# Performance work log

Measured on AMD Instinct MI355X. Metric: run time of the kernel, lower is better.

Reference implementation:

```python
import jax, jax.numpy as jnp
import numpy as np

L = 4      # num_decoders
D = 512    # d (model dim)
F = 512    # f (attention dim; must equal D for residual adds)
V = 32000  # vocab_size
S = 2048   # sequence length
EPS = 1e-5


def layer_norm(x, g, b):
    mu = jnp.mean(x, axis=-1, keepdims=True)
    var = jnp.var(x, axis=-1, keepdims=True)
    return (x - mu) * jax.lax.rsqrt(var + EPS) * g + b


def setup_inputs() -> dict:
    key = jax.random.key(0)
    ks = jax.random.split(key, 20)
    s = 0.02
    n = jax.random.normal
    return {
        "x":   n(ks[0], (S, D), jnp.float32),
        "Wq":  n(ks[1], (L, D, F), jnp.float32) * s,
        "bq":  jnp.zeros((L, F), jnp.float32),
        "Wk":  n(ks[2], (L, D, F), jnp.float32) * s,
        "bk":  jnp.zeros((L, F), jnp.float32),
        "Wv":  n(ks[3], (L, D, F), jnp.float32) * s,
        "bv":  jnp.zeros((L, F), jnp.float32),
        "Wp":  n(ks[4], (L, F, F), jnp.float32) * s,
        "bp":  jnp.zeros((L, F), jnp.float32),
        "g1":  1.0 + n(ks[5], (L, F), jnp.float32) * s,
        "be1": n(ks[6], (L, F), jnp.float32) * s,
        "W1":  n(ks[7], (L, F, 4 * F), jnp.float32) * s,
        "b1":  jnp.zeros((L, 4 * F), jnp.float32),
        "W2":  n(ks[8], (L, 4 * F, D), jnp.float32) * s,
        "b2":  jnp.zeros((L, D), jnp.float32),
        "g2":  1.0 + n(ks[9], (L, D), jnp.float32) * s,
        "be2": n(ks[10], (L, D), jnp.float32) * s,
        "Wf":  n(ks[11], (D, V), jnp.float32) * s,
        "bf":  jnp.zeros((V,), jnp.float32),
    }


def reference(x, Wq, bq, Wk, bk, Wv, bv, Wp, bp, g1, be1, W1, b1, W2, b2, g2, be2, Wf, bf):
    seq = x.shape[0]
    scale = 1.0 / jnp.sqrt(jnp.asarray(F, x.dtype))
    # causal mask: position i attends to j <= i (intended triu masking)
    causal = jnp.tril(jnp.ones((seq, seq), dtype=bool))
    neg_inf = jnp.asarray(-jnp.inf, x.dtype)
    for l in range(L):
        res = jax.lax.stop_gradient(x)  # original uses x.detach().clone()
        q = x @ Wq[l] + bq[l]
        k = x @ Wk[l] + bk[l]
        v = x @ Wv[l] + bv[l]
        scores = (q @ k.T) * scale                      # [S, S]
        scores = jnp.where(causal, scores, neg_inf)
        att = jax.nn.softmax(scores, axis=1)
        z = (att @ v) @ Wp[l] + bp[l]
        x = layer_norm(z + res, g1[l], be1[l])
        res = jax.lax.stop_gradient(x)
        h = x @ W1[l] + b1[l]                           # no activation in original FFN
        h = h @ W2[l] + b2[l]
        x = layer_norm(h + res, g2[l], be2[l])
    logits = x @ Wf + bf                                # [S, V]
    return jax.nn.softmax(logits, axis=1)
```

## Files before the change

### kernel.cpp

```cpp
#include <hip/hip_runtime.h>
#include <cmath>

#define SEQ 2048
#define DIM 512
#define FDIM 512
#define HDIM 2048
#define VOCAB 32000
#define NLAYER 4
#define LNEPS 1e-5f

typedef unsigned short ushort_t;
typedef __attribute__((ext_vector_type(8))) short short8;
typedef __attribute__((ext_vector_type(4))) float f32x4;

__device__ __forceinline__ ushort_t f2bf(float x) {
    union { float f; unsigned int u; } a; a.f = x;
    unsigned int r = a.u + 0x7fffu + ((a.u >> 16) & 1u);
    return (ushort_t)(r >> 16);
}
__device__ __forceinline__ float bf2f(ushort_t b) {
    union { unsigned int u; float f; } a; a.u = ((unsigned int)b) << 16; return a.f;
}

__device__ __forceinline__ void gload_lds16(const ushort_t* g, ushort_t* l) {
    __builtin_amdgcn_global_load_lds(
        (const __attribute__((address_space(1))) void*)g,
        (__attribute__((address_space(3))) void*)l, 16, 0, 0);
}

#define GEMM_CORE(AH, AL, BH, BL, LDA, LDB, KSTEPS, KBASE, TM, TN)                 \
    __shared__ ushort_t lds[16384];                                                \
    ushort_t* ldsAh = lds;                                                         \
    ushort_t* ldsAl = lds + 4096;                                                  \
    ushort_t* ldsBh = lds + 8192;                                                  \
    ushort_t* ldsBl = lds + 12288;                                                 \
    const int tid  = threadIdx.x;                                                  \
    const int lane = tid & 63, wv = tid >> 6;                                      \
    const int wm = wv >> 1, wn = wv & 1;                                           \
    const int q = lane >> 4, mlo = lane & 15;                                      \
    const int tm = (TM), tn = (TN);                                                \
    f32x4 acc[4][4];                                                               \
    _Pragma("unroll")                                                              \
    for (int i = 0; i < 4; i++)                                                    \
        _Pragma("unroll")                                                          \
        for (int j = 0; j < 4; j++)                                                \
            acc[i][j] = (f32x4){0.f, 0.f, 0.f, 0.f};                               \
    for (int ks = 0; ks < (KSTEPS); ks++) {                                        \
        const int k0 = (KBASE) + (ks << 5);                                        \
        _Pragma("unroll")                                                          \
        for (int r = 0; r < 2; r++) {                                              \
            const int c  = (r << 8) + (wv << 6) + lane;                            \
            const int i  = c & 127, kb = c >> 7;                                   \
            const int lofs = ((r << 8) + (wv << 6)) << 3;                          \
            const size_t aoff = (size_t)(tm + i) * (LDA) + k0 + (kb << 3);         \
            const size_t boff = (size_t)(tn + i) * (LDB) + k0 + (kb << 3);         \
            gload_lds16((AH) + aoff, ldsAh + lofs);                                \
            gload_lds16((AL) + aoff, ldsAl + lofs);                                \
            gload_lds16((BH) + boff, ldsBh + lofs);                                \
            gload_lds16((BL) + boff, ldsBl + lofs);                                \
        }                                                                          \
        __syncthreads();                                                           \
        short8 ah[4], al[4], bh[4], bl[4];                                         \
        _Pragma("unroll")                                                          \
        for (int t = 0; t < 4; t++) {                                              \
            const int ma = ((q << 7) + (wm << 6) + (t << 4) + mlo) << 3;           \
            const int nb = ((q << 7) + (wn << 6) + (t << 4) + mlo) << 3;           \
            ah[t] = *(const short8*)&ldsAh[ma];                                    \
            al[t] = *(const short8*)&ldsAl[ma];                                    \
            bh[t] = *(const short8*)&ldsBh[nb];                                    \
            bl[t] = *(const short8*)&ldsBl[nb];                                    \
        }                                                                          \
        _Pragma("unroll")                                                          \
        for (int i = 0; i < 4; i++)                                                \
            _Pragma("unroll")                                                      \
            for (int j = 0; j < 4; j++) {                                          \
                acc[i][j] = __builtin_amdgcn_mfma_f32_16x16x32_bf16(ah[i], bh[j], acc[i][j], 0, 0, 0); \
                acc[i][j] = __builtin_amdgcn_mfma_f32_16x16x32_bf16(ah[i], bl[j], acc[i][j], 0, 0, 0); \
                acc[i][j] = __builtin_amdgcn_mfma_f32_16x16x32_bf16(al[i], bh[j], acc[i][j], 0, 0, 0); \
            }                                                                      \
        __syncthreads();                                                           \
    }

__global__ __launch_bounds__(256) void gemm_bf16x3_k(
    const ushort_t* __restrict__ Ah, const ushort_t* __restrict__ Al,
    const ushort_t* __restrict__ Bh, const ushort_t* __restrict__ Bl,
    const float* __restrict__ bias, float* __restrict__ C,
    int K, int lda, int ldb, int ldc, float scale, int splitk, int flags,
    int bsA, int bsB, int bsC, int bsBias, int bsPart)
{
    const int bz = blockIdx.z;
    const int l  = bz / splitk, zz = bz - l * splitk;
    Ah += (size_t)l * bsA; Al += (size_t)l * bsA;
    Bh += (size_t)l * bsB; Bl += (size_t)l * bsB;
    C  += (size_t)l * bsC;
    if (bias != nullptr) bias += (size_t)l * bsBias;
    int bx = blockIdx.x, by = blockIdx.y;
    if (flags & 4) { const int t = bx; bx = by; by = t; }
    const int tmq = by << 7, tnq = bx << 7;
    if ((flags & 1) && tnq > tmq + 127) return;
    int ksteps = (K >> 5) / splitk;
    const int kbase = zz * ksteps * 32;
    if (flags & 2) {
        const int rem = (tmq + 128 - kbase) >> 5;
        if (rem < ksteps) ksteps = rem;
        if (ksteps <= 0) return;
    }
    GEMM_CORE(Ah, Al, Bh, Bl, lda, ldb, ksteps, kbase, tmq, tnq)
    const bool addb = (bias != nullptr) && (zz == 0);
    float* Cw = C + ((splitk > 1 && bsPart) ? (size_t)zz * bsPart : 0);
#pragma unroll
    for (int ti = 0; ti < 4; ti++)
#pragma unroll
        for (int tj = 0; tj < 4; tj++) {
            const int col = tn + (wn << 6) + (tj << 4) + mlo;
            const float bb = addb ? bias[col] : 0.f;
#pragma unroll
            for (int r = 0; r < 4; r++) {
                const int row = tm + (wm << 6) + (ti << 4) + (q << 2) + r;
                const float v = acc[ti][tj][r] * scale + bb;
                if (splitk == 1 || bsPart) Cw[(size_t)row * ldc + col] = v;
                else atomicAdd(&C[(size_t)row * ldc + col], v);
            }
        }
}

__global__ __launch_bounds__(256) void gemm_qkv_k(
    const ushort_t* __restrict__ Ah, const ushort_t* __restrict__ Al,
    const ushort_t* __restrict__ Bh, const ushort_t* __restrict__ Bl,
    const float* __restrict__ bias,
    ushort_t* __restrict__ QKh, ushort_t* __restrict__ QKl,
    ushort_t* __restrict__ Vh,  ushort_t* __restrict__ Vl)
{
    GEMM_CORE(Ah, Al, Bh, Bl, DIM, DIM, (DIM >> 5), 0,
              (int)(blockIdx.y << 7), (int)(blockIdx.x << 7))
#pragma unroll
    for (int ti = 0; ti < 4; ti++)
#pragma unroll
        for (int tj = 0; tj < 4; tj++) {
            const int col = tn + (wn << 6) + (tj << 4) + mlo;
            const float bb = bias[col];
#pragma unroll
            for (int r = 0; r < 4; r++) {
                const int row = tm + (wm << 6) + (ti << 4) + (q << 2) + r;
                const float v = acc[ti][tj][r] + bb;
                const ushort_t h = f2bf(v);
                const ushort_t lo = f2bf(v - bf2f(h));
                if (col < 1024) {
                    QKh[(size_t)row * 1024 + col] = h;
                    QKl[(size_t)row * 1024 + col] = lo;
                } else {
                    Vh[(size_t)(col - 1024) * SEQ + row] = h;
                    Vl[(size_t)(col - 1024) * SEQ + row] = lo;
                }
            }
        }
}

__global__ __launch_bounds__(128) void split_k(
    const float* __restrict__ src, int ld, int C,
    ushort_t* __restrict__ dh, ushort_t* __restrict__ dl)
{
    const int row = blockIdx.y;
    const int c4 = ((blockIdx.x << 7) + threadIdx.x) << 2;
    if (c4 >= C) return;
    const float4 v = *(const float4*)&src[(size_t)row * ld + c4];
    ushort_t h[4], l[4];
    const float f[4] = {v.x, v.y, v.z, v.w};
#pragma unroll
    for (int i = 0; i < 4; i++) {
        h[i] = f2bf(f[i]);
        l[i] = f2bf(f[i] - bf2f(h[i]));
    }
    *(ushort4*)&dh[(size_t)row * C + c4] = make_ushort4(h[0], h[1], h[2], h[3]);
    *(ushort4*)&dl[(size_t)row * C + c4] = make_ushort4(l[0], l[1], l[2], l[3]);
}

__global__ __launch_bounds__(128) void split_b_k(
    const float* __restrict__ src0, int ld, int C, int sbs,
    ushort_t* __restrict__ dh0, ushort_t* __restrict__ dl0, int dbs)
{
    const int lz = blockIdx.z;
    const float* src = src0 + (size_t)lz * sbs;
    ushort_t* dh = dh0 + (size_t)lz * dbs;
    ushort_t* dl = dl0 + (size_t)lz * dbs;
    const int row = blockIdx.y;
    const int c4 = ((blockIdx.x << 7) + threadIdx.x) << 2;
    if (c4 >= C) return;
    const float4 v = *(const float4*)&src[(size_t)row * ld + c4];
    ushort_t h[4], l[4];
    const float f[4] = {v.x, v.y, v.z, v.w};
#pragma unroll
    for (int i = 0; i < 4; i++) {
        h[i] = f2bf(f[i]);
        l[i] = f2bf(f[i] - bf2f(h[i]));
    }
    *(ushort4*)&dh[(size_t)row * C + c4] = make_ushort4(h[0], h[1], h[2], h[3]);
    *(ushort4*)&dl[(size_t)row * C + c4] = make_ushort4(l[0], l[1], l[2], l[3]);
}

__global__ __launch_bounds__(256) void tsplit_k(
    const float* __restrict__ src, int ld, int R,
    ushort_t* __restrict__ dh, ushort_t* __restrict__ dl)
{
    __shared__ float t[32][33];
    const int c = threadIdx.x & 31, r8 = threadIdx.x >> 5;
    const int bx = blockIdx.x, by = blockIdx.y;
#pragma unroll
    for (int i = 0; i < 4; i++) {
        const int r = (r8 << 2) + i;
        t[r][c] = src[(size_t)((by << 5) + r) * ld + (bx << 5) + c];
    }
    __syncthreads();
#pragma unroll
    for (int i = 0; i < 4; i++) {
        const int rr = (r8 << 2) + i;
        const float v = t[c][rr];
        const ushort_t h = f2bf(v);
        const ushort_t l = f2bf(v - bf2f(h));
        const size_t o = (size_t)((bx << 5) + rr) * R + (by << 5) + c;
        dh[o] = h; dl[o] = l;
    }
}

__global__ __launch_bounds__(256) void tsplit_b_k(
    const float* __restrict__ src0, int ld, int R, int sbs,
    ushort_t* __restrict__ dh0, ushort_t* __restrict__ dl0, int dbs)
{
    const int lz = blockIdx.z;
    const float* src = src0 + (size_t)lz * sbs;
    ushort_t* dh = dh0 + (size_t)lz * dbs;
    ushort_t* dl = dl0 + (size_t)lz * dbs;
    __shared__ float t[32][33];
    const int c = threadIdx.x & 31, r8 = threadIdx.x >> 5;
    const int bx = blockIdx.x, by = blockIdx.y;
#pragma unroll
    for (int i = 0; i < 4; i++) {
        const int r = (r8 << 2) + i;
        t[r][c] = src[(size_t)((by << 5) + r) * ld + (bx << 5) + c];
    }
    __syncthreads();
#pragma unroll
    for (int i = 0; i < 4; i++) {
        const int rr = (r8 << 2) + i;
        const float v = t[c][rr];
        const ushort_t h = f2bf(v);
        const ushort_t l = f2bf(v - bf2f(h));
        const size_t o = (size_t)((bx << 5) + rr) * R + (by << 5) + c;
        dh[o] = h; dl[o] = l;
    }
}

__global__ void gatherqkv_k(const float* bq, const float* bk, const float* bvp, float* d)
{
    const int i = blockIdx.x * 256 + threadIdx.x;
    if (i >= NLAYER * 1536) return;
    const int l = i / 1536, j = i - l * 1536;
    float v;
    if (j < 512)       v = bq[l * 512 + j];
    else if (j < 1024) v = bk[l * 512 + j - 512];
    else               v = bvp[l * 512 + j - 1024];
    d[i] = v;
}

__global__ __launch_bounds__(256) void bvecg_k(
    const float* __restrict__ vec, const float* __restrict__ W,
    float* __restrict__ outp, int sbsV, int sbsW)
{
    const int lz = blockIdx.z;
    vec  += (size_t)lz * sbsV;
    W    += (size_t)lz * sbsW;
    outp += (size_t)lz * DIM;
    const int c  = (blockIdx.x << 7) + (threadIdx.x & 127);
    const int h0 = (blockIdx.y << 7) + (threadIdx.x >> 7);
    float acc = 0.f;
#pragma unroll 8
    for (int i = 0; i < 64; i++) {
        const int h = h0 + (i << 1);
        acc += vec[h] * W[(size_t)h * DIM + c];
    }
    atomicAdd(&outp[c], acc);
}

__global__ __launch_bounds__(256) void softmax_causal_split_k(
    const float* __restrict__ sc, ushort_t* __restrict__ dh, ushort_t* __restrict__ dl)
{
    const int i = blockIdx.x;
    const float* p0 = sc + (size_t)i * SEQ;
    const float* p1 = p0 + (size_t)SEQ * SEQ;
    const int tid = threadIdx.x;
    __shared__ float red[4];
    const int base = tid << 2;
    const int lim = ((i >> 7) + 1) << 7;

    float4 v[2];
#pragma unroll
    for (int c = 0; c < 2; c++) {
        const int idx = (c << 10) + base;
        const float4 a = *(const float4*)&p0[idx];
        const float4 b = *(const float4*)&p1[idx];
        v[c].x = a.x + b.x; v[c].y = a.y + b.y;
        v[c].z = a.z + b.z; v[c].w = a.w + b.w;
    }

    float m = -3.402823466e38f;
#pragma unroll
    for (int c = 0; c < 2; c++) {
        float* f = (float*)&v[c];
        const int idx = (c << 10) + base;
#pragma unroll
        for (int j = 0; j < 4; j++) {
            if (idx + j > i) f[j] = -3.402823466e38f;
            m = fmaxf(m, f[j]);
        }
    }
#pragma unroll
    for (int o = 32; o > 0; o >>= 1) m = fmaxf(m, __shfl_down(m, o, 64));
    if ((tid & 63) == 0) red[tid >> 6] = m;
    __syncthreads();
    m = fmaxf(fmaxf(red[0], red[1]), fmaxf(red[2], red[3]));
    __syncthreads();

    float s = 0.f;
#pragma unroll
    for (int c = 0; c < 2; c++) {
        float* f = (float*)&v[c];
#pragma unroll
        for (int j = 0; j < 4; j++) {
            f[j] = expf(f[j] - m);
            s += f[j];
        }
    }
#pragma unroll
    for (int o = 32; o > 0; o >>= 1) s += __shfl_down(s, o, 64);
    if ((tid & 63) == 0) red[tid >> 6] = s;
    __syncthreads();
    const float inv = 1.0f / (red[0] + red[1] + red[2] + red[3]);

#pragma unroll
    for (int c = 0; c < 2; c++) {
        float* f = (float*)&v[c];
        const int idx = (c << 10) + base;
        if (idx >= lim) continue;
        ushort_t hp[4], lp[4];
#pragma unroll
        for (int j = 0; j < 4; j++) {
            const float e = f[j] * inv;
            hp[j] = f2bf(e);
            lp[j] = f2bf(e - bf2f(hp[j]));
        }
        *(ushort4*)&dh[(size_t)i * SEQ + idx] = make_ushort4(hp[0], hp[1], hp[2], hp[3]);
        *(ushort4*)&dl[(size_t)i * SEQ + idx] = make_ushort4(lp[0], lp[1], lp[2], lp[3]);
    }
}

__global__ __launch_bounds__(256) void add_ln_split_k(
    const float* __restrict__ zp, const float* __restrict__ res,
    const float* __restrict__ g, const float* __restrict__ b,
    float* __restrict__ outp, ushort_t* __restrict__ dh, ushort_t* __restrict__ dl,
    int parts, int clampk)
{
    const int row = blockIdx.x;
    const int tid = threadIdx.x;
    __shared__ float red[4];
    const size_t base = (size_t)row * DIM;
    const size_t pst  = (size_t)SEQ * DIM;
    int np = clampk ? ((row >> 9) + 1) : parts;
    if (np > parts) np = parts;
    float v0 = res[base + tid];
    float v1 = res[base + tid + 256];
    for (int p = 0; p < np; p++) {
        v0 += zp[(size_t)p * pst + base + tid];
        v1 += zp[(size_t)p * pst + base + tid + 256];
    }
    float s = v0 + v1;
#pragma unroll
    for (int o = 32; o > 0; o >>= 1) s += __shfl_down(s, o, 64);
    if ((tid & 63) == 0) red[tid >> 6] = s;
    __syncthreads();
    const float mean = (red[0] + red[1] + red[2] + red[3]) * (1.0f / DIM);
    __syncthreads();
    const float d0 = v0 - mean, d1 = v1 - mean;
    float vs = d0 * d0 + d1 * d1;
#pragma unroll
    for (int o = 32; o > 0; o >>= 1) vs += __shfl_down(vs, o, 64);
    if ((tid & 63) == 0) red[tid >> 6] = vs;
    __syncthreads();
    const float var = (red[0] + red[1] + red[2] + red[3]) * (1.0f / DIM);
    const float inv = 1.0f / sqrtf(var + LNEPS);
    const float o0 = d0 * inv * g[tid] + b[tid];
    const float o1 = d1 * inv * g[tid + 256] + b[tid + 256];
    outp[base + tid]       = o0;
    outp[base + tid + 256] = o1;
    const ushort_t h0 = f2bf(o0), h1 = f2bf(o1);
    dh[base + tid]       = h0;  dl[base + tid]       = f2bf(o0 - bf2f(h0));
    dh[base + tid + 256] = h1;  dl[base + tid + 256] = f2bf(o1 - bf2f(h1));
}

__global__ __launch_bounds__(1024) void softmax_rows_k(float* __restrict__ p)
{
    const int row = blockIdx.x;
    float* r = p + (size_t)row * VOCAB;
    const int tid = threadIdx.x;
    __shared__ float red[16];
    const int base = tid << 2;

    float4 v[8];
#pragma unroll
    for (int c = 0; c < 7; c++) v[c] = *(const float4*)&r[(c << 12) + base];
    const bool tail = (28672 + base) < VOCAB;
    if (tail) v[7] = *(const float4*)&r[28672 + base];
    else { v[7].x = v[7].y = v[7].z = v[7].w = -3.402823466e38f; }

    float m = -3.402823466e38f;
#pragma unroll
    for (int c = 0; c < 8; c++)
        m = fmaxf(m, fmaxf(fmaxf(v[c].x, v[c].y), fmaxf(v[c].z, v[c].w)));
#pragma unroll
    for (int o = 32; o > 0; o >>= 1) m = fmaxf(m, __shfl_down(m, o, 64));
    if ((tid & 63) == 0) red[tid >> 6] = m;
    __syncthreads();
    m = red[0];
#pragma unroll
    for (int w = 1; w < 16; w++) m = fmaxf(m, red[w]);
    __syncthreads();

    float s = 0.f;
#pragma unroll
    for (int c = 0; c < 8; c++) {
        float* f = (float*)&v[c];
#pragma unroll
        for (int j = 0; j < 4; j++) {
            f[j] = expf(f[j] - m);
            s += f[j];
        }
    }
#pragma unroll
    for (int o = 32; o > 0; o >>= 1) s += __shfl_down(s, o, 64);
    if ((tid & 63) == 0) red[tid >> 6] = s;
    __syncthreads();
    float tot = 0.f;
#pragma unroll
    for (int w = 0; w < 16; w++) tot += red[w];
    const float inv = 1.0f / tot;

#pragma unroll
    for (int c = 0; c < 7; c++) {
        float4 o4;
        o4.x = v[c].x * inv; o4.y = v[c].y * inv;
        o4.z = v[c].z * inv; o4.w = v[c].w * inv;
        *(float4*)&r[(c << 12) + base] = o4;
    }
    if (tail) {
        float4 o4;
        o4.x = v[7].x * inv; o4.y = v[7].y * inv;
        o4.z = v[7].z * inv; o4.w = v[7].w * inv;
        *(float4*)&r[28672 + base] = o4;
    }
}

extern "C" void kernel_launch(void* const* d_in, const int* in_sizes, int n_in,
                              void* d_out, int out_size, void* d_ws, size_t ws_size,
                              hipStream_t stream)
{
    const float* x   = (const float*)d_in[0];
    const float* Wq  = (const float*)d_in[1];
    const float* bq  = (const float*)d_in[2];
    const float* Wk  = (const float*)d_in[3];
    const float* bk  = (const float*)d_in[4];
    const float* Wv  = (const float*)d_in[5];
    const float* bv  = (const float*)d_in[6];
    const float* Wp  = (const float*)d_in[7];
    const float* bp  = (const float*)d_in[8];
    const float* g1  = (const float*)d_in[9];
    const float* be1 = (const float*)d_in[10];
    const float* W1  = (const float*)d_in[11];
    const float* b1  = (const float*)d_in[12];
    const float* W2  = (const float*)d_in[13];
    const float* b2  = (const float*)d_in[14];
    const float* g2  = (const float*)d_in[15];
    const float* be2 = (const float*)d_in[16];
    const float* Wf  = (const float*)d_in[17];
    const float* bf  = (const float*)d_in[18];
    float* out = (float*)d_out;

    char* ws = (char*)d_ws;
    auto alloc = [&](size_t bytes) {
        void* p = ws;
        ws += (bytes + 255) & ~(size_t)255;
        return p;
    };
    float*    x0     = (float*)alloc((size_t)SEQ * DIM * 4);
    float*    x1     = (float*)alloc((size_t)SEQ * DIM * 4);
    float*    z2p    = (float*)alloc((size_t)4 * SEQ * DIM * 4);
    float*    sc     = (float*)alloc((size_t)2 * SEQ * SEQ * 4);
    float*    PtA    = (float*)alloc((size_t)NLAYER * FDIM * DIM * 4);
    float*    WvpA   = (float*)alloc((size_t)NLAYER * FDIM * DIM * 4);
    ushort_t* QKh    = (ushort_t*)alloc((size_t)SEQ * 1024 * 2);
    ushort_t* QKl    = (ushort_t*)alloc((size_t)SEQ * 1024 * 2);
    ushort_t* X0h    = (ushort_t*)alloc((size_t)SEQ * DIM * 2);
    ushort_t* X0l    = (ushort_t*)alloc((size_t)SEQ * DIM * 2);
    ushort_t* X1h    = (ushort_t*)alloc((size_t)SEQ * DIM * 2);
    ushort_t* X1l    = (ushort_t*)alloc((size_t)SEQ * DIM * 2);
    ushort_t* AttH   = (ushort_t*)alloc((size_t)SEQ * SEQ * 2);
    ushort_t* AttL   = (ushort_t*)alloc((size_t)SEQ * SEQ * 2);
    ushort_t* Wbh    = (ushort_t*)alloc((size_t)NLAYER * 1536 * 512 * 2);
    ushort_t* Wbl    = (ushort_t*)alloc((size_t)NLAYER * 1536 * 512 * 2);
    ushort_t* WpTh   = (ushort_t*)alloc((size_t)NLAYER * 512 * 512 * 2);
    ushort_t* WpTl   = (ushort_t*)alloc((size_t)NLAYER * 512 * 512 * 2);
    ushort_t* Wvh    = (ushort_t*)alloc((size_t)NLAYER * 512 * 512 * 2);
    ushort_t* Wvl    = (ushort_t*)alloc((size_t)NLAYER * 512 * 512 * 2);
    ushort_t* W2th   = (ushort_t*)alloc((size_t)NLAYER * 512 * 2048 * 2);
    ushort_t* W2tl   = (ushort_t*)alloc((size_t)NLAYER * 512 * 2048 * 2);
    ushort_t* W1h    = (ushort_t*)alloc((size_t)NLAYER * 512 * 2048 * 2);
    ushort_t* W1l    = (ushort_t*)alloc((size_t)NLAYER * 512 * 2048 * 2);
    ushort_t* Pth    = (ushort_t*)alloc((size_t)NLAYER * 512 * 512 * 2);
    ushort_t* Ptl    = (ushort_t*)alloc((size_t)NLAYER * 512 * 512 * 2);
    ushort_t* VpTh   = (ushort_t*)alloc((size_t)FDIM * SEQ * 2);
    ushort_t* VpTl   = (ushort_t*)alloc((size_t)FDIM * SEQ * 2);
    ushort_t* Wfh    = (ushort_t*)alloc((size_t)VOCAB * DIM * 2);
    ushort_t* Wfl    = (ushort_t*)alloc((size_t)VOCAB * DIM * 2);
    float*    bqkvA  = (float*)alloc((size_t)NLAYER * 1536 * 4);
    float*    bvpA   = (float*)alloc((size_t)NLAYER * DIM * 4);
    float*    bvecA  = (float*)alloc((size_t)NLAYER * DIM * 4);

    const float att_scale = 1.0f / sqrtf((float)FDIM);
    const dim3 b256(256), b128(128), b1024(1024);

    hipMemcpyAsync(x0, x, (size_t)SEQ * DIM * 4, hipMemcpyDeviceToDevice, stream);
    tsplit_b_k<<<dim3(16, 16, NLAYER), b256, 0, stream>>>(Wq, FDIM, DIM, 262144, Wbh, Wbl, 786432);
    tsplit_b_k<<<dim3(16, 16, NLAYER), b256, 0, stream>>>(Wk, FDIM, DIM, 262144, Wbh + 262144, Wbl + 262144, 786432);
    tsplit_b_k<<<dim3(16, 16, NLAYER), b256, 0, stream>>>(Wp, FDIM, FDIM, 262144, WpTh, WpTl, 262144);
    split_k<<<dim3(1, NLAYER * 512), b128, 0, stream>>>(Wv, 512, 512, Wvh, Wvl);
    hipMemsetAsync(WvpA, 0, (size_t)NLAYER * FDIM * DIM * 4, stream);
    gemm_bf16x3_k<<<dim3(4, 4, NLAYER * 2), b256, 0, stream>>>(
        WpTh, WpTl, Wvh, Wvl, nullptr, WvpA, 512, 512, 512, 512, 1.0f, 2, 0,
        262144, 262144, 262144, 0, 0);
    split_b_k<<<dim3(1, 512, NLAYER), b128, 0, stream>>>(
        WvpA, 512, 512, 262144, Wbh + 524288, Wbl + 524288, 786432);
    hipMemsetAsync(bvpA, 0, (size_t)NLAYER * DIM * 4, stream);
    bvecg_k<<<dim3(4, 4, NLAYER), b256, 0, stream>>>(bv, Wp, bvpA, 512, 262144);
    tsplit_b_k<<<dim3(16, 64, NLAYER), b256, 0, stream>>>(W2, DIM, HDIM, HDIM * DIM, W2th, W2tl, 1048576);
    split_k<<<dim3(4, NLAYER * 512), b128, 0, stream>>>(W1, HDIM, HDIM, W1h, W1l);
    hipMemsetAsync(PtA, 0, (size_t)NLAYER * FDIM * DIM * 4, stream);
    gemm_bf16x3_k<<<dim3(4, 4, NLAYER * 8), b256, 0, stream>>>(
        W2th, W2tl, W1h, W1l, nullptr, PtA, HDIM, HDIM, HDIM, DIM, 1.0f, 8, 0,
        1048576, 1048576, 262144, 0, 0);
    split_k<<<dim3(1, NLAYER * 512), b128, 0, stream>>>(PtA, DIM, DIM, Pth, Ptl);
    hipMemcpyAsync(bvecA, b2, (size_t)NLAYER * DIM * 4, hipMemcpyDeviceToDevice, stream);
    bvecg_k<<<dim3(4, 16, NLAYER), b256, 0, stream>>>(b1, W2, bvecA, HDIM, HDIM * DIM);
    gatherqkv_k<<<dim3(24), b256, 0, stream>>>(bq, bk, bvpA, bqkvA);
    tsplit_k<<<dim3(VOCAB / 32, DIM / 32), b256, 0, stream>>>(Wf, VOCAB, DIM, Wfh, Wfl);
    split_k<<<dim3(1, SEQ), b128, 0, stream>>>(x0, DIM, DIM, X0h, X0l);

    for (int l = 0; l < NLAYER; l++) {
        gemm_qkv_k<<<dim3(12, 16), b256, 0, stream>>>(
            X0h, X0l, Wbh + (size_t)l * 786432, Wbl + (size_t)l * 786432,
            bqkvA + (size_t)l * 1536, QKh, QKl, VpTh, VpTl);

        gemm_bf16x3_k<<<dim3(16, 16, 2), b256, 0, stream>>>(
            QKh, QKl, QKh + 512, QKl + 512, nullptr, sc,
            FDIM, 1024, 1024, SEQ, att_scale, 2, 1, 0, 0, 0, 0, SEQ * SEQ);

        softmax_causal_split_k<<<dim3(SEQ), b256, 0, stream>>>(sc, AttH, AttL);

        gemm_bf16x3_k<<<dim3(4, 16, 4), b256, 0, stream>>>(
            AttH, AttL, VpTh, VpTl, bp + l * FDIM, z2p,
            SEQ, SEQ, SEQ, DIM, 1.0f, 4, 2, 0, 0, 0, 0, SEQ * DIM);

        add_ln_split_k<<<dim3(SEQ), b256, 0, stream>>>(
            z2p, x0, g1 + l * FDIM, be1 + l * FDIM, x1, X1h, X1l, 4, 1);

        gemm_bf16x3_k<<<dim3(4, 16, 4), b256, 0, stream>>>(
            X1h, X1l, Pth + (size_t)l * 262144, Ptl + (size_t)l * 262144,
            bvecA + (size_t)l * DIM, z2p, DIM, DIM, DIM, DIM, 1.0f, 4, 0,
            0, 0, 0, 0, SEQ * DIM);

        add_ln_split_k<<<dim3(SEQ), b256, 0, stream>>>(
            z2p, x1, g2 + l * DIM, be2 + l * DIM, x0, X0h, X0l, 4, 0);
    }

    gemm_bf16x3_k<<<dim3(SEQ / 128, VOCAB / 128, 1), b256, 0, stream>>>(
        X0h, X0l, Wfh, Wfl, bf, out, DIM, DIM, DIM, VOCAB, 1.0f, 1, 4,
        0, 0, 0, 0, 0);
    softmax_rows_k<<<dim3(SEQ), b1024, 0, stream>>>(out);
}
```

Measured before the change: 1.514 ms.

## Add XCD-aware workgroup remapping and deepen split-K for attention GEMMs

Measured after the change: 1.560 ms. 3.0% more time.

```diff
diff --git a/kernel.cpp b/kernel.cpp
--- a/kernel.cpp
+++ b/kernel.cpp
@@ -95,6 +95,15 @@
     C  += (size_t)l * bsC;
     if (bias != nullptr) bias += (size_t)l * bsBias;
     int bx = blockIdx.x, by = blockIdx.y;
+    if (flags & 8) {
+        const int gx = gridDim.x;
+        const int nwg = gx * gridDim.y;
+        const int flat = bx + gx * by;
+        const int qd = nwg >> 3, rm = nwg & 7;
+        const int xcd = flat & 7, loc = flat >> 3;
+        const int w = (xcd < rm ? xcd * (qd + 1) : rm * (qd + 1) + (xcd - rm) * qd) + loc;
+        bx = w % gx; by = w / gx;
+    }
     if (flags & 4) { const int t = bx; bx = by; by = t; }
     const int tmq = by << 7, tnq = bx << 7;
     if ((flags & 1) && tnq > tmq + 127) return;
@@ -286,20 +295,23 @@
 {
     const int i = blockIdx.x;
     const float* p0 = sc + (size_t)i * SEQ;
-    const float* p1 = p0 + (size_t)SEQ * SEQ;
     const int tid = threadIdx.x;
     __shared__ float red[4];
     const int base = tid << 2;
     const int lim = ((i >> 7) + 1) << 7;
+    const size_t pst = (size_t)SEQ * SEQ;
 
     float4 v[2];
 #pragma unroll
     for (int c = 0; c < 2; c++) {
         const int idx = (c << 10) + base;
-        const float4 a = *(const float4*)&p0[idx];
-        const float4 b = *(const float4*)&p1[idx];
-        v[c].x = a.x + b.x; v[c].y = a.y + b.y;
-        v[c].z = a.z + b.z; v[c].w = a.w + b.w;
+        float4 a = *(const float4*)&p0[idx];
+#pragma unroll
+        for (int p = 1; p < 4; p++) {
+            const float4 b = *(const float4*)&p0[(size_t)p * pst + idx];
+            a.x += b.x; a.y += b.y; a.z += b.z; a.w += b.w;
+        }
+        v[c] = a;
     }
 
     float m = -3.402823466e38f;
@@ -357,14 +369,14 @@
     const float* __restrict__ zp, const float* __restrict__ res,
     const float* __restrict__ g, const float* __restrict__ b,
     float* __restrict__ outp, ushort_t* __restrict__ dh, ushort_t* __restrict__ dl,
-    int parts, int clampk)
+    int parts, int shift)
 {
     const int row = blockIdx.x;
     const int tid = threadIdx.x;
     __shared__ float red[4];
     const size_t base = (size_t)row * DIM;
     const size_t pst  = (size_t)SEQ * DIM;
-    int np = clampk ? ((row >> 9) + 1) : parts;
+    int np = shift ? ((row >> shift) + 1) : parts;
     if (np > parts) np = parts;
     float v0 = res[base + tid];
     float v1 = res[base + tid + 256];
@@ -491,8 +503,8 @@
     };
     float*    x0     = (float*)alloc((size_t)SEQ * DIM * 4);
     float*    x1     = (float*)alloc((size_t)SEQ * DIM * 4);
-    float*    z2p    = (float*)alloc((size_t)4 * SEQ * DIM * 4);
-    float*    sc     = (float*)alloc((size_t)2 * SEQ * SEQ * 4);
+    float*    z2p    = (float*)alloc((size_t)8 * SEQ * DIM * 4);
+    float*    sc     = (float*)alloc((size_t)4 * SEQ * SEQ * 4);
     float*    PtA    = (float*)alloc((size_t)NLAYER * FDIM * DIM * 4);
     float*    WvpA   = (float*)alloc((size_t)NLAYER * FDIM * DIM * 4);
     ushort_t* QKh    = (ushort_t*)alloc((size_t)SEQ * 1024 * 2);
@@ -557,22 +569,22 @@
             X0h, X0l, Wbh + (size_t)l * 786432, Wbl + (size_t)l * 786432,
             bqkvA + (size_t)l * 1536, QKh, QKl, VpTh, VpTl);
 
-        gemm_bf16x3_k<<<dim3(16, 16, 2), b256, 0, stream>>>(
+        gemm_bf16x3_k<<<dim3(16, 16, 4), b256, 0, stream>>>(
             QKh, QKl, QKh + 512, QKl + 512, nullptr, sc,
-            FDIM, 1024, 1024, SEQ, att_scale, 2, 1, 0, 0, 0, 0, SEQ * SEQ);
+            FDIM, 1024, 1024, SEQ, att_scale, 4, 1 | 8, 0, 0, 0, 0, SEQ * SEQ);
 
         softmax_causal_split_k<<<dim3(SEQ), b256, 0, stream>>>(sc, AttH, AttL);
 
-        gemm_bf16x3_k<<<dim3(4, 16, 4), b256, 0, stream>>>(
+        gemm_bf16x3_k<<<dim3(4, 16, 8), b256, 0, stream>>>(
             AttH, AttL, VpTh, VpTl, bp + l * FDIM, z2p,
-            SEQ, SEQ, SEQ, DIM, 1.0f, 4, 2, 0, 0, 0, 0, SEQ * DIM);
+            SEQ, SEQ, SEQ, DIM, 1.0f, 8, 2 | 8, 0, 0, 0, 0, SEQ * DIM);
 
         add_ln_split_k<<<dim3(SEQ), b256, 0, stream>>>(
-            z2p, x0, g1 + l * FDIM, be1 + l * FDIM, x1, X1h, X1l, 4, 1);
+            z2p, x0, g1 + l * FDIM, be1 + l * FDIM, x1, X1h, X1l, 8, 8);
 
         gemm_bf16x3_k<<<dim3(4, 16, 4), b256, 0, stream>>>(
             X1h, X1l, Pth + (size_t)l * 262144, Ptl + (size_t)l * 262144,
-            bvecA + (size_t)l * DIM, z2p, DIM, DIM, DIM, DIM, 1.0f, 4, 0,
+            bvecA + (size_t)l * DIM, z2p, DIM, DIM, DIM, DIM, 1.0f, 4, 8,
             0, 0, 0, 0, SEQ * DIM);
 
         add_ln_split_k<<<dim3(SEQ), b256, 0, stream>>>(
@@ -580,7 +592,7 @@
     }
 
     gemm_bf16x3_k<<<dim3(SEQ / 128, VOCAB / 128, 1), b256, 0, stream>>>(
-        X0h, X0l, Wfh, Wfl, bf, out, DIM, DIM, DIM, VOCAB, 1.0f, 1, 4,
+        X0h, X0l, Wfh, Wfl, bf, out, DIM, DIM, DIM, VOCAB, 1.0f, 1, 4 | 8,
         0, 0, 0, 0, 0);
     softmax_rows_k<<<dim3(SEQ), b1024, 0, stream>>>(out);
 }
```
